# Kernel tuning notes

Measured on AMD Instinct MI355X. Metric: run time of the kernel, lower is better.

Reference implementation:

```python
import jax, jax.numpy as jnp
import numpy as np

N, E, D, EDGE_DIM = 50000, 150000, 100, 200

def _w(key, fi, fo):
    return jax.random.normal(key, (fi, fo), dtype=jnp.float32) / np.float32(np.sqrt(fi))

def setup_inputs():
    key = jax.random.key(0)
    ks = jax.random.split(key, 40)
    inp = {}
    inp["x"] = jax.random.normal(ks[0], (N, D), dtype=jnp.float32)
    inp["msg"] = jax.random.normal(ks[1], (E, D), dtype=jnp.float32)
    # TimeEncoder: Linear(1, D)
    inp["time_w"] = _w(ks[2], 1, D)
    inp["time_b"] = jnp.zeros((D,), jnp.float32)
    # TransformerConv 1: in=100, heads=8, out=100, concat -> 800
    H1 = 8 * D
    inp["c1_qw"] = _w(ks[3], D, H1); inp["c1_qb"] = jnp.zeros((H1,), jnp.float32)
    inp["c1_kw"] = _w(ks[4], D, H1); inp["c1_kb"] = jnp.zeros((H1,), jnp.float32)
    inp["c1_vw"] = _w(ks[5], D, H1); inp["c1_vb"] = jnp.zeros((H1,), jnp.float32)
    inp["c1_ew"] = _w(ks[6], EDGE_DIM, H1)  # lin_edge has no bias in PyG
    inp["c1_sw"] = _w(ks[7], D, H1); inp["c1_sb"] = jnp.zeros((H1,), jnp.float32)
    # TransformerConv 2: in=800, heads=1, out=100, concat=False
    inp["c2_qw"] = _w(ks[8], H1, D); inp["c2_qb"] = jnp.zeros((D,), jnp.float32)
    inp["c2_kw"] = _w(ks[9], H1, D); inp["c2_kb"] = jnp.zeros((D,), jnp.float32)
    inp["c2_vw"] = _w(ks[10], H1, D); inp["c2_vb"] = jnp.zeros((D,), jnp.float32)
    inp["c2_ew"] = _w(ks[11], EDGE_DIM, D)
    inp["c2_sw"] = _w(ks[12], H1, D); inp["c2_sb"] = jnp.zeros((D,), jnp.float32)
    # LinkPredictor (in_channels=100, out=2)
    inp["lp_src_w"] = _w(ks[13], D, 2 * D); inp["lp_src_b"] = jnp.zeros((2 * D,), jnp.float32)
    inp["lp_dst_w"] = _w(ks[14], D, 2 * D); inp["lp_dst_b"] = jnp.zeros((2 * D,), jnp.float32)
    inp["lp1_w"] = _w(ks[15], 4 * D, 8 * D); inp["lp1_b"] = jnp.zeros((8 * D,), jnp.float32)
    inp["lp2_w"] = _w(ks[16], 8 * D, 2 * D); inp["lp2_b"] = jnp.zeros((2 * D,), jnp.float32)
    inp["lp3_w"] = _w(ks[17], 2 * D, D // 2); inp["lp3_b"] = jnp.zeros((D // 2,), jnp.float32)
    inp["lp4_w"] = _w(ks[18], D // 2, 2); inp["lp4_b"] = jnp.zeros((2,), jnp.float32)
    inp["last_update"] = jax.random.randint(ks[19], (N,), 0, 1000000)
    inp["t"] = jax.random.randint(ks[20], (E,), 0, 1000000)
    inp["edge_index"] = jax.random.randint(ks[21], (2, E), 0, N)
    return inp

def _tconv(x, src, dst, edge_attr, qw, qb, kw, kb, vw, vb, ew, sw, sb, heads, out_ch, concat, n):
    q = (x @ qw + qb).reshape(n, heads, out_ch)
    k = (x @ kw + kb).reshape(n, heads, out_ch)
    v = (x @ vw + vb).reshape(n, heads, out_ch)
    e = (edge_attr @ ew).reshape(-1, heads, out_ch)        # [E,H,C]
    kj = k[src] + e                                        # gather src keys + edge
    alpha = jnp.sum(q[dst] * kj, axis=-1) / np.float32(np.sqrt(out_ch))  # [E,H]
    amax = jax.ops.segment_max(alpha, dst, num_segments=n)
    ex = jnp.exp(alpha - amax[dst])
    denom = jax.ops.segment_sum(ex, dst, num_segments=n)
    a = ex / (denom[dst] + 1e-16)                          # per-dest softmax
    agg = jax.ops.segment_sum((v[src] + e) * a[..., None], dst, num_segments=n)
    out = agg.reshape(n, heads * out_ch) if concat else jnp.mean(agg, axis=1)
    return out + x @ sw + sb                               # root/skip connection

def reference(x, msg, time_w, time_b,
              c1_qw, c1_qb, c1_kw, c1_kb, c1_vw, c1_vb, c1_ew, c1_sw, c1_sb,
              c2_qw, c2_qb, c2_kw, c2_kb, c2_vw, c2_vb, c2_ew, c2_sw, c2_sb,
              lp_src_w, lp_src_b, lp_dst_w, lp_dst_b,
              lp1_w, lp1_b, lp2_w, lp2_b, lp3_w, lp3_b, lp4_w, lp4_b,
              last_update, t, edge_index):
    src, dst = edge_index[0], edge_index[1]
    rel_t = (last_update[src] - t).astype(jnp.float32)[:, None]  # [E,1]
    rel_enc = jnp.cos(rel_t @ time_w + time_b)                   # [E,D]
    edge_attr = jnp.concatenate([rel_enc, msg], axis=-1)         # [E,200]
    h = jax.nn.relu(_tconv(x, src, dst, edge_attr, c1_qw, c1_qb, c1_kw, c1_kb,
                           c1_vw, c1_vb, c1_ew, c1_sw, c1_sb, 8, D, True, N))
    h = jax.nn.relu(_tconv(h, src, dst, edge_attr, c2_qw, c2_qb, c2_kw, c2_kb,
                           c2_vw, c2_vb, c2_ew, c2_sw, c2_sb, 1, D, False, N))
    hh = jnp.concatenate([h[src] @ lp_src_w + lp_src_b,
                          h[dst] @ lp_dst_w + lp_dst_b], axis=-1)
    hh = jnp.tanh(hh @ lp1_w + lp1_b)
    hh = jnp.tanh(hh @ lp2_w + lp2_b)
    hh = jnp.tanh(hh @ lp3_w + lp3_b)
    return hh @ lp4_w + lp4_b
```

## Files before the change

kernel.cpp:

```cpp
#include <hip/hip_runtime.h>
#include <hip/hip_bf16.h>
#include <math.h>

typedef __hip_bfloat16 bf16;
typedef short s16x8 __attribute__((ext_vector_type(8)));
typedef float f32x4 __attribute__((ext_vector_type(4)));

#define NN 50000
#define EE 150000
#define EH 75000

static __device__ __forceinline__ float b2f(bf16 x){ return __bfloat162float(x); }
static __device__ __forceinline__ bf16 f2b(float x){ return __float2bfloat16(x); }
static __device__ __forceinline__ short f2s(float x){
  union { bf16 b; short s; } u; u.b = f2b(x); return u.s;
}
static __device__ __forceinline__ float u2f_lo(unsigned u){ union{unsigned i;float f;}c; c.i=u<<16; return c.f; }
static __device__ __forceinline__ float u2f_hi(unsigned u){ union{unsigned i;float f;}c; c.i=u&0xffff0000u; return c.f; }

static __device__ __forceinline__ float fast_tanh(float x){
  float a = fabsf(x);
  float e = __expf(2.0f*a);
  float t = 1.0f - __fdividef(2.0f, e + 1.0f);
  return x < 0.f ? -t : t;
}

static __device__ __forceinline__ void gload_lds16(const void* g, void* l){
  __builtin_amdgcn_global_load_lds((const __attribute__((address_space(1))) void*)g,
                                   (__attribute__((address_space(3))) void*)l, 16, 0, 0);
}

template<int N> static __device__ __forceinline__ void wait_vmcnt(){
  if constexpr(N==0) asm volatile("s_waitcnt vmcnt(0)" ::: "memory");
  else if constexpr(N==1) asm volatile("s_waitcnt vmcnt(1)" ::: "memory");
  else if constexpr(N==2) asm volatile("s_waitcnt vmcnt(2)" ::: "memory");
  else if constexpr(N==3) asm volatile("s_waitcnt vmcnt(3)" ::: "memory");
  else if constexpr(N==4) asm volatile("s_waitcnt vmcnt(4)" ::: "memory");
  else if constexpr(N==5) asm volatile("s_waitcnt vmcnt(5)" ::: "memory");
  else asm volatile("s_waitcnt vmcnt(6)" ::: "memory");
}
static __device__ __forceinline__ void wait_lgkm0(){
  asm volatile("s_waitcnt lgkmcnt(0)" ::: "memory");
}
static __device__ __forceinline__ void memfence(){
  asm volatile("" ::: "memory");
}

__global__ void k_zero(int* __restrict__ p, int n){
  int i = blockIdx.x*blockDim.x + threadIdx.x;
  if(i<n) p[i]=0;
}

__global__ void k_hist(const int* __restrict__ dst, int* __restrict__ deg){
  int i = blockIdx.x*blockDim.x + threadIdx.x;
  if(i<EE) atomicAdd(&deg[dst[i]], 1);
}

__global__ void k_scan(const int* __restrict__ deg, int* __restrict__ rowptr){
  __shared__ int part[1024];
  int tid = threadIdx.x;
  const int n = NN;
  int chunk = (n + 1023)/1024;
  int start = tid*chunk;
  int end = start + chunk; if(end > n) end = n;
  int s = 0;
  for(int i=start;i<end;i++) s += deg[i];
  part[tid] = s; __syncthreads();
  for(int off=1; off<1024; off<<=1){
    int v = (tid>=off)? part[tid-off] : 0;
    __syncthreads();
    part[tid] += v;
    __syncthreads();
  }
  int run = (tid==0)? 0 : part[tid-1];
  for(int i=start;i<end;i++){ rowptr[i]=run; run += deg[i]; }
  if(tid==0) rowptr[n] = part[1023];
}

__global__ void k_scatter(const int* __restrict__ dst, const int* __restrict__ srcv,
                          const int* __restrict__ rowptr,
                          int* __restrict__ cursor, int* __restrict__ elist,
                          int* __restrict__ ssrc){
  int e = blockIdx.x*blockDim.x + threadIdx.x;
  if(e<EE){
    int d=dst[e]; int p=atomicAdd(&cursor[d],1);
    int pos = rowptr[d]+p;
    elist[pos]=e; ssrc[pos]=srcv[e];
  }
}

__global__ void k_relenc(const int* __restrict__ src, const int* __restrict__ tt,
                         const int* __restrict__ lu, const float* __restrict__ tw,
                         const float* __restrict__ tb, bf16* __restrict__ rel){
  int i = blockIdx.x*blockDim.x + threadIdx.x;
  if(i >= EE*112) return;
  int e = i/112, c = i - e*112;
  float v = 0.f;
  if(c < 100){
    float rt  = (float)(lu[src[e]] - tt[e]);
    float arg = __fadd_rn(__fmul_rn(rt, tw[c]), tb[c]);
    v = cosf(arg);
  }
  rel[i] = f2b(v);
}

__global__ void k_cvtpad(const float* __restrict__ in, int incols,
                         bf16* __restrict__ outp, int outcols, int total){
  int i = blockIdx.x*blockDim.x + threadIdx.x;
  if(i >= total) return;
  int r = i/outcols, c = i - r*outcols;
  outp[i] = f2b(c < incols ? in[(size_t)r*incols + c] : 0.f);
}

__global__ void k_wt2(const float* __restrict__ W, int K, int N, int colofs, int ncols,
                      bf16* __restrict__ WT, int kpad, int nrows){
  int i = blockIdx.x*blockDim.x + threadIdx.x;
  if(i >= nrows*kpad) return;
  int n = i / kpad, k = i - n*kpad;
  float v = (n<ncols && k<K)? W[(size_t)k*N + colofs + n] : 0.f;
  WT[i] = f2b(v);
}

__global__ void k_wtc1(const float* __restrict__ qw, const float* __restrict__ kw,
                       const float* __restrict__ vw, bf16* __restrict__ outp){
  int i = blockIdx.x*blockDim.x + threadIdx.x;
  if(i >= 8*320*128) return;
  int h = i/(320*128), r = (i/128)%320, k = i&127;
  float v = 0.f;
  if(r < 300 && k < 100){
    int s = r/100, n = r - s*100;
    const float* W = s==0? qw : s==1? kw : vw;
    v = W[(size_t)k*800 + h*100 + n];
  }
  outp[i] = f2b(v);
}

__global__ void k_wte(const float* __restrict__ ew, int N, int colofs,
                      bf16* __restrict__ outp){
  int i = blockIdx.x*blockDim.x + threadIdx.x;
  if(i >= 112*256) return;
  int r = i>>8, k = i&255;
  float v = 0.f;
  if(r < 100){
    if(k < 100) v = ew[(size_t)k*N + colofs + r];
    else if(k >= 128 && k < 228) v = ew[(size_t)(k-28)*N + colofs + r];
  }
  outp[i] = f2b(v);
}

__global__ void k_bstack3(const float* __restrict__ b0, const float* __restrict__ b1,
                          const float* __restrict__ b2, int W, int H,
                          float* __restrict__ outp){
  int i = blockIdx.x*blockDim.x + threadIdx.x;
  if(i >= H*3*W) return;
  int h = i/(3*W), r = i - h*3*W, s = r/W, c = r - s*W;
  const float* b = s==0? b0 : s==1? b1 : b2;
  outp[i] = b[h*W + c];
}

__global__ void k_foldw(const float* __restrict__ sw, const float* __restrict__ dw,
                        const float* __restrict__ w1, bf16* __restrict__ o){
  int i = blockIdx.x*blockDim.x + threadIdx.x;
  if(i >= 800*224) return;
  int n = i/224, k = i - n*224;
  float s = 0.f;
  if(k < 100){
    for(int j=0;j<200;j++) s += sw[k*200+j]*w1[(size_t)j*800+n];
  } else if(k >= 112 && k < 212){
    int kk = k-112;
    for(int j=0;j<200;j++) s += dw[kk*200+j]*w1[(size_t)(200+j)*800+n];
  }
  o[i] = f2b(s);
}
__global__ void k_foldb(const float* __restrict__ sb, const float* __restrict__ db,
                        const float* __restrict__ w1, const float* __restrict__ b1,
                        float* __restrict__ o){
  int n = blockIdx.x*blockDim.x + threadIdx.x;
  if(n >= 800) return;
  float s = b1[n];
  for(int j=0;j<200;j++) s += sb[j]*w1[(size_t)j*800+n] + db[j]*w1[(size_t)(200+j)*800+n];
  o[n] = s;
}

template<int NT>
static __device__ void mm_body(
    char* lds, int bx, int nstrip,
    const bf16* __restrict__ A1, int lda1, int kv1, const int* __restrict__ g1,
    int KS,
    const bf16* __restrict__ A2b, int lda2b, int kv2b, const int* __restrict__ g2,
    const float* __restrict__ A2f, int lda2f, int kv2f,
    const bf16* __restrict__ WT, int kpad,
    const bf16* __restrict__ zbuf,
    const float* __restrict__ bias,
    bf16* __restrict__ C, int ldc,
    int M, int nvalid, int act)
{
  constexpr int BN = NT*16;
  constexpr int BPASS = (BN*4 + 255)/256;
  constexpr int ABYTES = 8192;
  constexpr int BUFSZ = ABYTES + BPASS*4096;

  const int tid  = threadIdx.x;
  const int wave = tid>>6, lane = tid&63;
  const int quad = lane>>4, lo = lane&15;
  WT += (size_t)nstrip*BN*kpad;
  C  += (size_t)nstrip*BN;
  if(bias) bias += nstrip*BN;
  const int nval = nvalid - nstrip*BN;
  const int row0 = bx*128;

  float bvr[NT];
#pragma unroll
  for(int n=0;n<NT;n++){
    int col = n*16 + lo;
    bvr[n] = (bias && col < nval) ? bias[col] : 0.f;
  }
#pragma unroll
  for(int n=0;n<NT;n++) asm volatile("" :: "v"(bvr[n]));

  const char*  a1b[2];
  const char*  a2bp[2];
  const float* f2base[2];
  int acol0[2];
#pragma unroll
  for(int p=0;p<2;p++){
    int s = p*256 + tid;
    int row = s>>2, cp = s&3;
    int q = cp ^ ((row>>1)&3);
    int col0 = q*8;
    int rg = row0 + row; if(rg > M-1) rg = M-1;
    int r1 = g1 ? g1[rg] : rg;
    int r2 = g2 ? g2[rg] : rg;
    acol0[p] = col0;
    a1b[p]   = (const char*)A1 + ((size_t)r1*lda1 + col0)*2;
    a2bp[p]  = A2b ? (const char*)A2b + ((size_t)r2*lda2b)*2 : nullptr;
    f2base[p]= A2f ? (A2f + (size_t)r2*lda2f) : nullptr;
  }
  const char* bbase[BPASS];
#pragma unroll
  for(int p=0;p<BPASS;p++){
    int s = p*256 + tid;
    int rb = s>>2; if(rb > BN-1) rb = BN-1;
    int cp = s&3;
    int lq = cp ^ ((rb>>1)&3);
    bbase[p] = (const char*)WT + ((size_t)rb*kpad + lq*8)*2;
  }

  f32x4 acc[2][NT];
#pragma unroll
  for(int m=0;m<2;m++)
#pragma unroll
    for(int n=0;n<NT;n++) acc[m][n] = (f32x4){0.f,0.f,0.f,0.f};

  float4 pf0[2], pf1[2];

  auto stageA1 = [&](char* buf, int kb){
#pragma unroll
    for(int p=0;p<2;p++){
      int k = kb + acol0[p];
      const char* s;
      if(k < KS) s = (k < kv1) ? (a1b[p] + (size_t)kb*2) : (const char*)zbuf;
      else { int o = k - KS; s = (o < kv2b) ? (a2bp[p] + (size_t)o*2) : (const char*)zbuf; }
      gload_lds16(s, buf + p*4096 + wave*1024);
    }
  };
  auto loadA2f = [&](int kb){
#pragma unroll
    for(int p=0;p<2;p++){
      int o = kb + acol0[p] - KS;
      const float* ap = f2base[p] + o;
      pf0[p] = (o   < kv2f) ? *(const float4*)ap     : (float4){0.f,0.f,0.f,0.f};
      pf1[p] = (o+4 < kv2f) ? *(const float4*)(ap+4) : (float4){0.f,0.f,0.f,0.f};
    }
  };
  auto writeA2 = [&](char* buf){
#pragma unroll
    for(int p=0;p<2;p++){
      s16x8 v;
      v[0]=f2s(pf0[p].x); v[1]=f2s(pf0[p].y); v[2]=f2s(pf0[p].z); v[3]=f2s(pf0[p].w);
      v[4]=f2s(pf1[p].x); v[5]=f2s(pf1[p].y); v[6]=f2s(pf1[p].z); v[7]=f2s(pf1[p].w);
      *(s16x8*)(buf + p*4096 + (size_t)tid*16) = v;
    }
  };
  auto stageB = [&](char* buf, int kb){
#pragma unroll
    for(int p=0;p<BPASS;p++)
      gload_lds16(bbase[p] + (size_t)kb*2, buf + ABYTES + p*4096 + wave*1024);
  };
  auto compute = [&](const char* buf){
    s16x8 af[2];
#pragma unroll
    for(int m=0;m<2;m++){
      int rl = wave*32 + m*16 + lo;
      int cp = quad ^ ((rl>>1)&3);
      af[m] = *(const s16x8*)(buf + rl*64 + cp*16);
    }
#pragma unroll
    for(int n=0;n<NT;n++){
      int rb = n*16 + lo;
      int cp = quad ^ ((rb>>1)&3);
      s16x8 bfr = *(const s16x8*)(buf + ABYTES + rb*64 + cp*16);
      acc[0][n] = __builtin_amdgcn_mfma_f32_16x16x32_bf16(af[0], bfr, acc[0][n], 0,0,0);
      acc[1][n] = __builtin_amdgcn_mfma_f32_16x16x32_bf16(af[1], bfr, acc[1][n], 0,0,0);
    }
  };

  const int T = kpad >> 5;
  stageA1(lds, 0); stageB(lds, 0);
  if(T > 1){ stageA1(lds + BUFSZ, 32); stageB(lds + BUFSZ, 32); }

  for(int t=0; t<T; t++){
    bool nb  = (t+1 < T);
    bool nfp = nb && A2f && (((t+1)<<5) >= KS);
    if(!nb)      wait_vmcnt<0>();
    else if(nfp) wait_vmcnt<BPASS>();
    else         wait_vmcnt<2+BPASS>();
    wait_lgkm0();
    __builtin_amdgcn_s_barrier();
    memfence();
    int tp = t+2;
    bool sp  = (tp < T);
    bool spf = sp && A2f && ((tp<<5) >= KS);
    char* nb3 = lds + (tp%3)*BUFSZ;
    if(sp){
      int kb2 = tp<<5;
      if(spf) loadA2f(kb2);
      else    stageA1(nb3, kb2);
      stageB(nb3, kb2);
    }
    compute(lds + (t%3)*BUFSZ);
    if(spf) writeA2(nb3);
  }

  const int r0 = (lane&1)<<1;
#pragma unroll
  for(int n=0;n<NT;n++){
    int col  = n*16 + lo;
    int pcol = col & ~1;
    bool cok = (pcol < nval);
    float bv = bvr[n];
#pragma unroll
    for(int m=0;m<2;m++){
      float v[4];
#pragma unroll
      for(int r=0;r<4;r++){
        float t = acc[m][n][r] + bv;
        if(act==1) t = fmaxf(t, 0.f);
        else if(act==2) t = fast_tanh(t);
        v[r] = t;
      }
      unsigned mylo = (unsigned)(unsigned short)f2s(v[r0])
                    | ((unsigned)(unsigned short)f2s(v[r0+1])<<16);
      unsigned snd  = (unsigned)(unsigned short)f2s(v[r0^2])
                    | ((unsigned)(unsigned short)f2s(v[(r0^2)+1])<<16);
      unsigned got  = (unsigned)__shfl_xor((int)snd, 1);
      unsigned w0, w1;
      if(lane&1){ w0 = (got & 0xffffu) | (mylo<<16); w1 = (got>>16) | (mylo & 0xffff0000u); }
      else      { w0 = (mylo & 0xffffu) | (got<<16); w1 = (mylo>>16) | (got & 0xffff0000u); }
      if(cok){
        int prow = row0 + wave*32 + m*16 + quad*4 + r0;
        if(prow   < M) *(unsigned*)(C + (size_t)prow*ldc + pcol) = w0;
        if(prow+1 < M) *(unsigned*)(C + (size_t)(prow+1)*ldc + pcol) = w1;
      }
    }
  }
}

template<int NT>
__global__ __launch_bounds__(256) void mm_tile(
    const bf16* A1, int lda1, int kv1, const int* g1, int KS,
    const bf16* A2b, int lda2b, int kv2b, const int* g2,
    const float* A2f, int lda2f, int kv2f,
    const bf16* WT, int kpad, const bf16* zbuf, const float* bias,
    bf16* C, int ldc, int M, int nvalid, int act)
{
  constexpr int BUFSZ = 8192 + ((NT*16*4+255)/256)*4096;
  __shared__ __align__(16) char lds[3*BUFSZ];
  mm_body<NT>(lds, blockIdx.x, blockIdx.y, A1,lda1,kv1,g1, KS,
              A2b,lda2b,kv2b,g2, A2f,lda2f,kv2f, WT,kpad, zbuf, bias,
              C,ldc, M,nvalid,act);
}

__global__ __launch_bounds__(256) void k_attn(
    const int* __restrict__ rowptr, const int* __restrict__ ssrc,
    const bf16* __restrict__ qkv, const bf16* __restrict__ ehc,
    bf16* __restrict__ hout, int ldh, int colofs, int zpad)
{
  int wave = threadIdx.x>>6, lane = threadIdx.x&63;
  int node = blockIdx.x*4 + wave;
  if(node >= NN) return;
  bool act = (lane < 50);
  float q0=0.f, q1=0.f;
  const unsigned* qrow = (const unsigned*)(qkv + (size_t)node*300);
  if(act){ unsigned u = qrow[lane]; q0=u2f_lo(u); q1=u2f_hi(u); }
  int s0 = rowptr[node], s1 = rowptr[node+1];
  float m = -3.4e38f, d = 0.f, a0 = 0.f, a1 = 0.f;
  for(int j=s0; j<s1; j++){
    int sn = ssrc[j];
    float p = 0.f, e0=0.f, e1=0.f;
    if(act){
      unsigned uk = ((const unsigned*)(qkv + (size_t)sn*300 + 100))[lane];
      unsigned ue = ((const unsigned*)(ehc + (size_t)j*100))[lane];
      e0=u2f_lo(ue); e1=u2f_hi(ue);
      p = q0*(u2f_lo(uk)+e0) + q1*(u2f_hi(uk)+e1);
    }
    for(int off=32; off; off>>=1) p += __shfl_xor(p, off);
    float alpha = p * 0.1f;
    float mn = fmaxf(m, alpha);
    float sc = __expf(m - mn);
    float wv = __expf(alpha - mn);
    d = d*sc + wv;
    if(act){
      unsigned uv = ((const unsigned*)(qkv + (size_t)sn*300 + 200))[lane];
      a0 = a0*sc + wv*(u2f_lo(uv)+e0);
      a1 = a1*sc + wv*(u2f_hi(uv)+e1);
    }
    m = mn;
  }
  if(act){
    float inv = 1.f/(d + 1e-16f);
    unsigned us = ((const unsigned*)(hout + (size_t)node*ldh + colofs))[lane];
    float h0 = fmaxf(u2f_lo(us) + a0*inv, 0.f);
    float h1 = fmaxf(u2f_hi(us) + a1*inv, 0.f);
    bf16* op = hout + (size_t)node*ldh + colofs + lane*2;
    op[0] = f2b(h0); op[1] = f2b(h1);
  } else if(zpad && lane < 56){
    bf16* op = hout + (size_t)node*ldh + colofs + lane*2;
    op[0] = f2b(0.f); op[1] = f2b(0.f);
  }
}

__global__ void k_lpout(const bf16* __restrict__ t3, const float* __restrict__ w4,
                        const float* __restrict__ b4, float* __restrict__ out,
                        int base, int n){
  int i = blockIdx.x*blockDim.x + threadIdx.x;
  if(i >= n*2) return;
  int g = i>>1, j = i&1;
  const bf16* tp = t3 + (size_t)g*50;
  float s = 0.f;
  for(int k=0;k<50;k++) s += b2f(tp[k])*w4[k*2+j];
  out[(size_t)(base+g)*2 + j] = s + b4[j];
}

extern "C" void kernel_launch(void* const* d_in, const int* in_sizes, int n_in,
                              void* d_out, int out_size, void* d_ws, size_t ws_size,
                              hipStream_t stream){
  const float* x       = (const float*)d_in[0];
  const float* msg     = (const float*)d_in[1];
  const float* time_w  = (const float*)d_in[2];
  const float* time_b  = (const float*)d_in[3];
  const float* c1_qw=(const float*)d_in[4];  const float* c1_qb=(const float*)d_in[5];
  const float* c1_kw=(const float*)d_in[6];  const float* c1_kb=(const float*)d_in[7];
  const float* c1_vw=(const float*)d_in[8];  const float* c1_vb=(const float*)d_in[9];
  const float* c1_ew=(const float*)d_in[10];
  const float* c1_sw=(const float*)d_in[11]; const float* c1_sb=(const float*)d_in[12];
  const float* c2_qw=(const float*)d_in[13]; const float* c2_qb=(const float*)d_in[14];
  const float* c2_kw=(const float*)d_in[15]; const float* c2_kb=(const float*)d_in[16];
  const float* c2_vw=(const float*)d_in[17]; const float* c2_vb=(const float*)d_in[18];
  const float* c2_ew=(const float*)d_in[19];
  const float* c2_sw=(const float*)d_in[20]; const float* c2_sb=(const float*)d_in[21];
  const float* lp_src_w=(const float*)d_in[22]; const float* lp_src_b=(const float*)d_in[23];
  const float* lp_dst_w=(const float*)d_in[24]; const float* lp_dst_b=(const float*)d_in[25];
  const float* lp1_w=(const float*)d_in[26]; const float* lp1_b=(const float*)d_in[27];
  const float* lp2_w=(const float*)d_in[28]; const float* lp2_b=(const float*)d_in[29];
  const float* lp3_w=(const float*)d_in[30]; const float* lp3_b=(const float*)d_in[31];
  const float* lp4_w=(const float*)d_in[32]; const float* lp4_b=(const float*)d_in[33];
  const int* last_update=(const int*)d_in[34];
  const int* tt =(const int*)d_in[35];
  const int* edge_index=(const int*)d_in[36];
  const int* src = edge_index;
  const int* dst = edge_index + EE;
  float* out = (float*)d_out;

  char* ws = (char*)d_ws;
  bf16*  h1    = (bf16*) (ws + 0);
  bf16*  relpad= (bf16*) (ws + 80000000);
  bf16*  ehc   = (bf16*) (ws + 113600000);
  bf16*  qkv   = (bf16*) (ws + 143600000);
  bf16*  h2p   = (bf16*) (ws + 183600000);
  bf16*  xb    = (bf16*) (ws + 183600000);
  int*   rowptr= (int*)  (ws + 194800000);
  int*   elist = (int*)  (ws + 195000064);
  int*   ssrc  = (int*)  (ws + 195600064);
  int*   deg   = (int*)  (ws + 196200064);
  int*   cursor= (int*)  (ws + 196400064);
  bf16* c1all  = (bf16*)(ws + 196600064);
  bf16* c1eall = (bf16*)(ws + 197255424);
  bf16* c1swt  = (bf16*)(ws + 197714176);
  bf16* c2all  = (bf16*)(ws + 197918976);
  bf16* c2swt  = (bf16*)(ws + 198430976);
  bf16* c2e    = (bf16*)(ws + 198610176);
  bf16* lp1tF  = (bf16*)(ws + 198667520);
  bf16* lp2t   = (bf16*)(ws + 199025920);
  bf16* lp3t   = (bf16*)(ws + 199384320);
  float* c1ball= (float*)(ws + 199412992);
  float* c2ball= (float*)(ws + 199422592);
  float* lp1c  = (float*)(ws + 199423808);
  bf16* zbuf   = (bf16*)(ws + 199427008);
  bf16* lt1 = (bf16*)(ws + 0);
  bf16* lt2 = (bf16*)(ws + 120000000);
  bf16* lt3 = (bf16*)(ws + 150000000);

  k_wtc1<<<(8*320*128+255)/256,256,0,stream>>>(c1_qw,c1_kw,c1_vw,c1all);
  for(int h=0; h<8; h++)
    k_wte<<<(112*256+255)/256,256,0,stream>>>(c1_ew, 800, h*100, c1eall + (size_t)h*112*256);
  k_wte<<<(112*256+255)/256,256,0,stream>>>(c2_ew, 100, 0, c2e);
  k_wt2<<<(800*128+255)/256,256,0,stream>>>(c1_sw,100,800,0,800,c1swt,128,800);
  k_wt2<<<(100*800+255)/256,256,0,stream>>>(c2_qw,800,100,0,100,c2all,         800,100);
  k_wt2<<<(100*800+255)/256,256,0,stream>>>(c2_kw,800,100,0,100,c2all+100*800, 800,100);
  k_wt2<<<(100*800+255)/256,256,0,stream>>>(c2_vw,800,100,0,100,c2all+200*800, 800,100);
  k_wt2<<<(20*800+255)/256,256,0,stream>>>(c2_qw,800,100,0,0,   c2all+300*800, 800,20);
  k_wt2<<<(112*800+255)/256,256,0,stream>>>(c2_sw,800,100,0,100,c2swt,800,112);
  k_wt2<<<(224*800+255)/256,256,0,stream>>>(lp2_w,800,200,0,200,lp2t,800,224);
  k_wt2<<<(64*224+255)/256,256,0,stream>>>(lp3_w,200,50,0,50,lp3t,224,64);
  k_foldw<<<(800*224+255)/256,256,0,stream>>>(lp_src_w, lp_dst_w, lp1_w, lp1tF);
  k_foldb<<<(800+255)/256,256,0,stream>>>(lp_src_b, lp_dst_b, lp1_w, lp1_b, lp1c);
  k_bstack3<<<(8*300+255)/256,256,0,stream>>>(c1_qb,c1_kb,c1_vb,100,8,c1ball);
  k_bstack3<<<(300+255)/256,256,0,stream>>>(c2_qb,c2_kb,c2_vb,100,1,c2ball);
  k_zero<<<1,64,0,stream>>>((int*)zbuf, 16);
  k_cvtpad<<<(NN*112+255)/256,256,0,stream>>>(x, 100, xb, 112, NN*112);

  k_zero   <<<(NN+255)/256, 256, 0, stream>>>(deg, NN);
  k_zero   <<<(NN+255)/256, 256, 0, stream>>>(cursor, NN);
  k_hist   <<<(EE+255)/256, 256, 0, stream>>>(dst, deg);
  k_scan   <<<1, 1024, 0, stream>>>(deg, rowptr);
  k_scatter<<<(EE+255)/256, 256, 0, stream>>>(dst, src, rowptr, cursor, elist, ssrc);

  k_relenc<<<(EE*112+255)/256, 256, 0, stream>>>(src, tt, last_update, time_w, time_b, relpad);

  int gN = (NN + 127)/128;
  int gE = (EE + 127)/128;
  int gL = (EH + 127)/128;
  int gA = (NN + 3)/4;

  mm_tile<10><<<dim3(gN,5),256,0,stream>>>(xb,112,112,nullptr, 128,
      nullptr,0,0,nullptr, nullptr,0,0,
      c1swt,128, zbuf, c1_sb, h1,800, NN,800,0);

  for(int h=0; h<8; h++){
    mm_tile<10><<<dim3(gN,2),256,0,stream>>>(xb,112,112,nullptr, 128,
        nullptr,0,0,nullptr, nullptr,0,0,
        c1all + (size_t)h*320*128, 128, zbuf, c1ball + h*300, qkv,300, NN,300,0);
    mm_tile<7><<<dim3(gE,1),256,0,stream>>>(relpad,112,112,elist, 128,
        nullptr,0,0,elist, msg,100,100,
        c1eall + (size_t)h*112*256, 256, zbuf, nullptr, ehc,100, EE,100,0);
    k_attn<<<gA,256,0,stream>>>(rowptr, ssrc, qkv, ehc, h1, 800, h*100, 0);
  }

  mm_tile<10><<<dim3(gN,2),256,0,stream>>>(h1,800,800,nullptr, 800,
      nullptr,0,0,nullptr, nullptr,0,0,
      c2all,800, zbuf, c2ball, qkv,300, NN,300,0);
  mm_tile<7><<<dim3(gE,1),256,0,stream>>>(relpad,112,112,elist, 128,
      nullptr,0,0,elist, msg,100,100,
      c2e,256, zbuf, nullptr, ehc,100, EE,100,0);
  mm_tile<7><<<dim3(gN,1),256,0,stream>>>(h1,800,800,nullptr, 800,
      nullptr,0,0,nullptr, nullptr,0,0,
      c2swt,800, zbuf, c2_sb, h2p,112, NN,100,0);
  k_attn<<<gA,256,0,stream>>>(rowptr, ssrc, qkv, ehc, h2p, 112, 0, 1);

  for(int half=0; half<2; half++){
    const int* esrc = src + half*EH;
    const int* edst = dst + half*EH;
    mm_tile<10><<<dim3(gL,5),256,0,stream>>>(h2p,112,112,esrc, 112,
        h2p,112,112,edst, nullptr,0,0,
        lp1tF,224, zbuf, lp1c, lt1,800, EH,800,2);
    mm_tile<7><<<dim3(gL,2),256,0,stream>>>(lt1,800,800,nullptr, 800,
        nullptr,0,0,nullptr, nullptr,0,0,
        lp2t,800, zbuf, lp2_b, lt2,200, EH,200,2);
    mm_tile<4><<<dim3(gL,1),256,0,stream>>>(lt2,200,200,nullptr, 224,
        nullptr,0,0,nullptr, nullptr,0,0,
        lp3t,224, zbuf, lp3_b, lt3,50, EH,50,2);
    k_lpout<<<(EH*2+255)/256,256,0,stream>>>(lt3, lp4_w, lp4_b, out, half*EH, EH);
  }

  (void)in_sizes; (void)n_in; (void)out_size; (void)ws_size;
}
```

Baseline: 2.054 ms.

## Store relenc in CSR order and add register-preloaded gather GEMM for link predictor

The relative-time encoding is now written in dst-sorted (elist) order, so the edge GEMMs read it contiguously rather than through an index gather. The msg half is still gathered via elist. A new mm_gath kernel for the first link-predictor layer loads all gathered src/dst A rows into registers up front and streams only the weights through a triple-buffered LDS pipeline. This removes gather indirection and LDS staging of A, at the cost of higher register pressure.

```diff
diff --git a/kernel.cpp b/kernel.cpp
--- a/kernel.cpp
+++ b/kernel.cpp
@@ -89,15 +89,17 @@
   }
 }
 
-__global__ void k_relenc(const int* __restrict__ src, const int* __restrict__ tt,
-                         const int* __restrict__ lu, const float* __restrict__ tw,
-                         const float* __restrict__ tb, bf16* __restrict__ rel){
+__global__ void k_relenc(const int* __restrict__ elist, const int* __restrict__ ssrc,
+                         const int* __restrict__ tt, const int* __restrict__ lu,
+                         const float* __restrict__ tw, const float* __restrict__ tb,
+                         bf16* __restrict__ rel){
   int i = blockIdx.x*blockDim.x + threadIdx.x;
   if(i >= EE*112) return;
-  int e = i/112, c = i - e*112;
+  int j = i/112, c = i - j*112;
   float v = 0.f;
   if(c < 100){
-    float rt  = (float)(lu[src[e]] - tt[e]);
+    int e = elist[j];
+    float rt  = (float)(lu[ssrc[j]] - tt[e]);
     float arg = __fadd_rn(__fmul_rn(rt, tw[c]), tb[c]);
     v = cosf(arg);
   }
@@ -379,6 +381,137 @@
   mm_body<NT>(lds, blockIdx.x, blockIdx.y, A1,lda1,kv1,g1, KS,
               A2b,lda2b,kv2b,g2, A2f,lda2f,kv2f, WT,kpad, zbuf, bias,
               C,ldc, M,nvalid,act);
+}
+
+template<int NT>
+__global__ __launch_bounds__(256) void mm_gath(
+    const bf16* __restrict__ A, int lda, int KS,
+    const int* __restrict__ gs, const int* __restrict__ gd,
+    const bf16* __restrict__ WT,
+    const float* __restrict__ bias,
+    bf16* __restrict__ C, int ldc,
+    int M, int nvalid, int act)
+{
+  constexpr int T = 7;
+  constexpr int KPAD = 224;
+  constexpr int BN = NT*16;
+  constexpr int BPASS = (BN*4 + 255)/256;
+  constexpr int BUFSZ = BPASS*4096;
+  __shared__ __align__(16) char lds[3*BUFSZ];
+
+  const int tid  = threadIdx.x;
+  const int wave = tid>>6, lane = tid&63;
+  const int quad = lane>>4, lo = lane&15;
+  const int nstrip = blockIdx.y;
+  const bf16* WTs = WT + (size_t)nstrip*BN*KPAD;
+  C += (size_t)nstrip*BN;
+  const float* bp = bias ? bias + nstrip*BN : nullptr;
+  const int nval = nvalid - nstrip*BN;
+  const int row0 = blockIdx.x*128;
+
+  float bvr[NT];
+#pragma unroll
+  for(int n=0;n<NT;n++){
+    int col = n*16 + lo;
+    bvr[n] = (bp && col < nval) ? bp[col] : 0.f;
+  }
+
+  const bf16* abase[2][2];
+#pragma unroll
+  for(int m=0;m<2;m++){
+    int r = row0 + wave*32 + m*16 + lo; if(r > M-1) r = M-1;
+    abase[m][0] = A + (size_t)gs[r]*lda;
+    abase[m][1] = A + (size_t)gd[r]*lda;
+  }
+
+  s16x8 areg[T][2];
+#pragma unroll
+  for(int t=0;t<T;t++){
+#pragma unroll
+    for(int m=0;m<2;m++){
+      int k = t*32 + quad*8;
+      const bf16* p = (k < KS) ? (abase[m][0] + k) : (abase[m][1] + (k - KS));
+      asm volatile("global_load_dwordx4 %0, %1, off"
+                   : "=v"(areg[t][m]) : "v"(p));
+    }
+  }
+  memfence();
+
+  const char* bbase[BPASS];
+#pragma unroll
+  for(int p=0;p<BPASS;p++){
+    int s = p*256 + tid;
+    int rb = s>>2; if(rb > BN-1) rb = BN-1;
+    int cp = s&3;
+    int lq = cp ^ ((rb>>1)&3);
+    bbase[p] = (const char*)WTs + ((size_t)rb*KPAD + lq*8)*2;
+  }
+  auto stageB = [&](char* buf, int kb){
+#pragma unroll
+    for(int p=0;p<BPASS;p++)
+      gload_lds16(bbase[p] + (size_t)kb*2, buf + p*4096 + wave*1024);
+  };
+
+  f32x4 acc[2][NT];
+#pragma unroll
+  for(int m=0;m<2;m++)
+#pragma unroll
+    for(int n=0;n<NT;n++) acc[m][n] = (f32x4){0.f,0.f,0.f,0.f};
+
+  stageB(lds, 0);
+  stageB(lds + BUFSZ, 32);
+
+#pragma unroll
+  for(int t=0; t<T; t++){
+    if(t < T-1) wait_vmcnt<BPASS>();
+    else        wait_vmcnt<0>();
+    wait_lgkm0();
+    __builtin_amdgcn_s_barrier();
+    memfence();
+    if(t+2 < T) stageB(lds + ((t+2)%3)*BUFSZ, (t+2)*32);
+    const char* buf = lds + (t%3)*BUFSZ;
+#pragma unroll
+    for(int n=0;n<NT;n++){
+      int rb = n*16 + lo;
+      int cp = quad ^ ((rb>>1)&3);
+      s16x8 bfr = *(const s16x8*)(buf + rb*64 + cp*16);
+      acc[0][n] = __builtin_amdgcn_mfma_f32_16x16x32_bf16(areg[t][0], bfr, acc[0][n], 0,0,0);
+      acc[1][n] = __builtin_amdgcn_mfma_f32_16x16x32_bf16(areg[t][1], bfr, acc[1][n], 0,0,0);
+    }
+  }
+
+  const int r0 = (lane&1)<<1;
+#pragma unroll
+  for(int n=0;n<NT;n++){
+    int col  = n*16 + lo;
+    int pcol = col & ~1;
+    bool cok = (pcol < nval);
+    float bv = bvr[n];
+#pragma unroll
+    for(int m=0;m<2;m++){
+      float v[4];
+#pragma unroll
+      for(int r=0;r<4;r++){
+        float t = acc[m][n][r] + bv;
+        if(act==1) t = fmaxf(t, 0.f);
+        else if(act==2) t = fast_tanh(t);
+        v[r] = t;
+      }
+      unsigned mylo = (unsigned)(unsigned short)f2s(v[r0])
+                    | ((unsigned)(unsigned short)f2s(v[r0+1])<<16);
+      unsigned snd  = (unsigned)(unsigned short)f2s(v[r0^2])
+                    | ((unsigned)(unsigned short)f2s(v[(r0^2)+1])<<16);
+      unsigned got  = (unsigned)__shfl_xor((int)snd, 1);
+      unsigned w0, w1;
+      if(lane&1){ w0 = (got & 0xffffu) | (mylo<<16); w1 = (got>>16) | (mylo & 0xffff0000u); }
+      else      { w0 = (mylo & 0xffffu) | (got<<16); w1 = (mylo>>16) | (got & 0xffff0000u); }
+      if(cok){
+        int prow = row0 + wave*32 + m*16 + quad*4 + r0;
+        if(prow   < M) *(unsigned*)(C + (size_t)prow*ldc + pcol) = w0;
+        if(prow+1 < M) *(unsigned*)(C + (size_t)(prow+1)*ldc + pcol) = w1;
+      }
+    }
+  }
 }
 
 __global__ __launch_bounds__(256) void k_attn(
@@ -474,7 +607,7 @@
 
   char* ws = (char*)d_ws;
   bf16*  h1    = (bf16*) (ws + 0);
-  bf16*  relpad= (bf16*) (ws + 80000000);
+  bf16*  relc  = (bf16*) (ws + 80000000);
   bf16*  ehc   = (bf16*) (ws + 113600000);
   bf16*  qkv   = (bf16*) (ws + 143600000);
   bf16*  h2p   = (bf16*) (ws + 183600000);
@@ -526,7 +659,8 @@
   k_scan   <<<1, 1024, 0, stream>>>(deg, rowptr);
   k_scatter<<<(EE+255)/256, 256, 0, stream>>>(dst, src, rowptr, cursor, elist, ssrc);
 
-  k_relenc<<<(EE*112+255)/256, 256, 0, stream>>>(src, tt, last_update, time_w, time_b, relpad);
+  k_relenc<<<(EE*112+255)/256, 256, 0, stream>>>(elist, ssrc, tt, last_update,
+                                                 time_w, time_b, relc);
 
   int gN = (NN + 127)/128;
   int gE = (EE + 127)/128;
@@ -541,7 +675,7 @@
     mm_tile<10><<<dim3(gN,2),256,0,stream>>>(xb,112,112,nullptr, 128,
         nullptr,0,0,nullptr, nullptr,0,0,
         c1all + (size_t)h*320*128, 128, zbuf, c1ball + h*300, qkv,300, NN,300,0);
-    mm_tile<7><<<dim3(gE,1),256,0,stream>>>(relpad,112,112,elist, 128,
+    mm_tile<7><<<dim3(gE,1),256,0,stream>>>(relc,112,112,nullptr, 128,
         nullptr,0,0,elist, msg,100,100,
         c1eall + (size_t)h*112*256, 256, zbuf, nullptr, ehc,100, EE,100,0);
     k_attn<<<gA,256,0,stream>>>(rowptr, ssrc, qkv, ehc, h1, 800, h*100, 0);
@@ -550,7 +684,7 @@
   mm_tile<10><<<dim3(gN,2),256,0,stream>>>(h1,800,800,nullptr, 800,
       nullptr,0,0,nullptr, nullptr,0,0,
       c2all,800, zbuf, c2ball, qkv,300, NN,300,0);
-  mm_tile<7><<<dim3(gE,1),256,0,stream>>>(relpad,112,112,elist, 128,
+  mm_tile<7><<<dim3(gE,1),256,0,stream>>>(relc,112,112,nullptr, 128,
       nullptr,0,0,elist, msg,100,100,
       c2e,256, zbuf, nullptr, ehc,100, EE,100,0);
   mm_tile<7><<<dim3(gN,1),256,0,stream>>>(h1,800,800,nullptr, 800,
@@ -561,9 +695,8 @@
   for(int half=0; half<2; half++){
     const int* esrc = src + half*EH;
     const int* edst = dst + half*EH;
-    mm_tile<10><<<dim3(gL,5),256,0,stream>>>(h2p,112,112,esrc, 112,
-        h2p,112,112,edst, nullptr,0,0,
-        lp1tF,224, zbuf, lp1c, lt1,800, EH,800,2);
+    mm_gath<10><<<dim3(gL,5),256,0,stream>>>(h2p,112,112, esrc, edst,
+        lp1tF, lp1c, lt1,800, EH,800,2);
     mm_tile<7><<<dim3(gL,2),256,0,stream>>>(lt1,800,800,nullptr, 800,
         nullptr,0,0,nullptr, nullptr,0,0,
         lp2t,800, zbuf, lp2_b, lt2,200, EH,200,2);
```

Result: faster. 1.972 ms (-4.0%).
